# Optimization experiments

Hardware: AMD Instinct MI355X
Metric: run time of the kernel (lower is better)

## Reference

```python
import jax, jax.numpy as jnp
import numpy as np

H_MODEL = 1024
N_HEADS = 16
N_KV_HEADS = 4
HEAD_DIM = 64
SLIDING_WINDOW = 512
B, S = 2, 2048
NEG_INF = -1e9


def rotate_half(x):
    half = x.shape[-1] // 2
    return jnp.concatenate([-x[..., half:], x[..., :half]], axis=-1)


def setup_inputs() -> dict:
    key = jax.random.key(0)
    ks = jax.random.split(key, 8)
    hidden_states = jax.random.normal(ks[0], (B, S, H_MODEL), dtype=jnp.float32)
    # RoPE tables (HF style): cos/sin of shape [1, S, head_dim]
    inv_freq = 1.0 / (10000.0 ** (jnp.arange(0, HEAD_DIM, 2, dtype=jnp.float32) / HEAD_DIM))
    pos = jnp.arange(S, dtype=jnp.float32)
    freqs = jnp.einsum('s,d->sd', pos, inv_freq)            # [S, D/2]
    emb = jnp.concatenate([freqs, freqs], axis=-1)          # [S, D]
    cos = jnp.cos(emb)[None]                                # [1, S, D]
    sin = jnp.sin(emb)[None]
    # additive causal + sliding-window mask [1,1,S,S]
    i = jnp.arange(S)[:, None]
    j = jnp.arange(S)[None, :]
    allowed = (j <= i) & (i - j < SLIDING_WINDOW)
    attention_mask = jnp.where(allowed, 0.0, NEG_INF).astype(jnp.float32)[None, None]
    # projection weights (torch Linear stores [out, in]; y = x @ W.T)
    std = 0.02
    Wq = jax.random.normal(ks[1], (N_HEADS * HEAD_DIM, H_MODEL), dtype=jnp.float32) * std
    Wk = jax.random.normal(ks[2], (N_KV_HEADS * HEAD_DIM, H_MODEL), dtype=jnp.float32) * std
    Wv = jax.random.normal(ks[3], (N_KV_HEADS * HEAD_DIM, H_MODEL), dtype=jnp.float32) * std
    Wo = jax.random.normal(ks[4], (H_MODEL, N_HEADS * HEAD_DIM), dtype=jnp.float32) * std
    return {"hidden_states": hidden_states, "cos": cos, "sin": sin,
            "attention_mask": attention_mask, "Wq": Wq, "Wk": Wk, "Wv": Wv, "Wo": Wo}


def reference(hidden_states, cos, sin, attention_mask, Wq, Wk, Wv, Wo):
    b, s, _ = hidden_states.shape
    G = N_HEADS // N_KV_HEADS
    scaling = HEAD_DIM ** -0.5
    # QKV projections -> [B, H, S, D]
    q = jnp.einsum('bsh,oh->bso', hidden_states, Wq).reshape(b, s, N_HEADS, HEAD_DIM).transpose(0, 2, 1, 3)
    k = jnp.einsum('bsh,oh->bso', hidden_states, Wk).reshape(b, s, N_KV_HEADS, HEAD_DIM).transpose(0, 2, 1, 3)
    v = jnp.einsum('bsh,oh->bso', hidden_states, Wv).reshape(b, s, N_KV_HEADS, HEAD_DIM).transpose(0, 2, 1, 3)
    # RoPE (cos/sin broadcast over head dim via unsqueeze(1))
    c = cos[:, None, :, :]
    sn = sin[:, None, :, :]
    q = q * c + rotate_half(q) * sn
    k = k * c + rotate_half(k) * sn
    # GQA eager attention: group query heads over kv heads
    qg = q.reshape(b, N_KV_HEADS, G, s, HEAD_DIM)
    scores = jnp.einsum('bkgqd,bkpd->bkgqp', qg, k) * scaling  # [B,Hkv,G,S,S]
    scores = scores + attention_mask[:, :, None, :, :]
    probs = jax.nn.softmax(scores.astype(jnp.float32), axis=-1).astype(q.dtype)
    out = jnp.einsum('bkgqp,bkpd->bkgqd', probs, v)            # [B,Hkv,G,S,D]
    out = out.reshape(b, N_HEADS, s, HEAD_DIM).transpose(0, 2, 1, 3).reshape(b, s, N_HEADS * HEAD_DIM)
    return jnp.einsum('bso,ho->bsh', out, Wo)
```

## Files before the change

### kernel.cpp

```cpp
#include <hip/hip_runtime.h>
#include <hip/hip_bf16.h>

#define S_LEN 2048
#define NH 16
#define NKV 4
#define HD 64
#define WIN 512
#define BATCH 2

typedef __bf16 bf16_8 __attribute__((ext_vector_type(8)));
typedef __bf16 bf16_4 __attribute__((ext_vector_type(4)));
typedef float f32x4 __attribute__((ext_vector_type(4)));

__device__ inline void gld16(const __bf16* g, __bf16* l) {
    __builtin_amdgcn_global_load_lds(
        (const __attribute__((address_space(1))) void*)g,
        (__attribute__((address_space(3))) void*)l, 16, 0, 0);
}

__device__ inline bf16_8 cvt8(f32x4 a, f32x4 b) {
    bf16_8 r;
    r[0] = (__bf16)a[0]; r[1] = (__bf16)a[1]; r[2] = (__bf16)a[2]; r[3] = (__bf16)a[3];
    r[4] = (__bf16)b[0]; r[5] = (__bf16)b[1]; r[6] = (__bf16)b[2]; r[7] = (__bf16)b[3];
    return r;
}

__global__ __launch_bounds__(256) void cvt_w(
    const float* __restrict__ s0, const float* __restrict__ s1,
    const float* __restrict__ s2, const float* __restrict__ s3,
    __bf16* __restrict__ d0, __bf16* __restrict__ d1,
    __bf16* __restrict__ d2, __bf16* __restrict__ d3,
    int c0, int c1, int c2, int c3)
{
    const int i = blockIdx.x * blockDim.x + threadIdx.x;
    if (i >= c3) return;
    const float* s; __bf16* d; int base;
    if (i < c0)      { s = s0; d = d0; base = 0;  }
    else if (i < c1) { s = s1; d = d1; base = c0; }
    else if (i < c2) { s = s2; d = d2; base = c1; }
    else             { s = s3; d = d3; base = c2; }
    const size_t j = (size_t)(i - base) * 4;
    const f32x4 v = *(const f32x4*)(s + j);
    bf16_4 o;
    o[0] = (__bf16)v[0]; o[1] = (__bf16)v[1];
    o[2] = (__bf16)v[2]; o[3] = (__bf16)v[3];
    *(bf16_4*)(d + j) = o;
}

__global__ __launch_bounds__(256) void gemm_qkv(
    const float* __restrict__ A,
    const __bf16* __restrict__ Wqb,
    const __bf16* __restrict__ Wkb,
    const __bf16* __restrict__ Wvb,
    __bf16* __restrict__ Qb,
    __bf16* __restrict__ Kb,
    __bf16* __restrict__ Vt,
    const float* __restrict__ cosb,
    const float* __restrict__ sinb)
{
    __shared__ __align__(16) __bf16 As[64 * 32];
    __shared__ __align__(16) __bf16 Bs[128 * 32];

    const int tid  = threadIdx.x;
    const int wave = tid >> 6;
    const int lane = tid & 63;
    const int wm   = wave & 1;
    const int wn   = wave >> 1;

    const int row0 = blockIdx.x * 64;
    const int by   = blockIdx.y;

    const __bf16* B; int colb; int mode;
    __bf16* C; int ldc; int col0;
    if (by < 8)       { B = Wqb; colb = by * 128;        C = Qb; ldc = 1024; col0 = by * 128;        mode = 0; }
    else if (by < 10) { B = Wkb; colb = (by - 8) * 128;  C = Kb; ldc = 256;  col0 = (by - 8) * 128;  mode = 1; }
    else              { B = Wvb; colb = (by - 10) * 128; C = 0;  ldc = 0;    col0 = (by - 10) * 128; mode = 2; }

    const int arow = tid >> 2;
    const int akc  = (tid & 3) << 3;
    const int srow = lane >> 2;
    const int skc  = (lane & 3) << 3;

    const int fm = lane & 15;
    const int fk = (lane >> 4) << 3;

    const f32x4 fzero = {0.f, 0.f, 0.f, 0.f};
    f32x4 acc[2][4];
#pragma unroll
    for (int i = 0; i < 2; ++i)
#pragma unroll
        for (int nt = 0; nt < 4; ++nt) acc[i][nt] = fzero;

    for (int k0 = 0; k0 < 1024; k0 += 32) {
        const f32x4 x0 = *(const f32x4*)&A[(size_t)(row0 + arow) * 1024 + k0 + akc];
        const f32x4 x1 = *(const f32x4*)&A[(size_t)(row0 + arow) * 1024 + k0 + akc + 4];
#pragma unroll
        for (int s = 0; s < 2; ++s) {
            const int ch = 2 * wave + s;
            gld16(&B[(size_t)(colb + ch * 16 + srow) * 1024 + k0 + skc],
                  &Bs[ch * 16 * 32]);
        }
        *(bf16_8*)&As[arow * 32 + akc] = cvt8(x0, x1);
        __syncthreads();

        bf16_8 af[2], bfr[4];
#pragma unroll
        for (int i = 0; i < 2; ++i)
            af[i] = *(const bf16_8*)&As[(wm * 32 + i * 16 + fm) * 32 + fk];
#pragma unroll
        for (int nt = 0; nt < 4; ++nt)
            bfr[nt] = *(const bf16_8*)&Bs[(wn * 64 + nt * 16 + fm) * 32 + fk];
#pragma unroll
        for (int i = 0; i < 2; ++i)
#pragma unroll
            for (int nt = 0; nt < 4; ++nt)
                acc[i][nt] = __builtin_amdgcn_mfma_f32_16x16x32_bf16(af[i], bfr[nt], acc[i][nt], 0, 0, 0);
        __syncthreads();
    }

    const int drow = (lane >> 4) << 2;
    const int cq   = col0 + wn * 64;
    if (mode < 2) {
#pragma unroll
        for (int i = 0; i < 2; ++i) {
#pragma unroll
            for (int r = 0; r < 4; ++r) {
                const int row = row0 + wm * 32 + i * 16 + drow + r;
                const int s   = row & (S_LEN - 1);
#pragma unroll
                for (int nt = 0; nt < 2; ++nt) {
                    const int d = nt * 16 + fm;
                    const float c1 = cosb[s * HD + d];
                    const float s1 = sinb[s * HD + d];
                    const float c2 = cosb[s * HD + d + 32];
                    const float s2 = sinb[s * HD + d + 32];
                    const float x1 = acc[i][nt][r];
                    const float x2 = acc[i][nt + 2][r];
                    C[(size_t)row * ldc + cq + d]      = (__bf16)(x1 * c1 - x2 * s1);
                    C[(size_t)row * ldc + cq + d + 32] = (__bf16)(x2 * c2 + x1 * s2);
                }
            }
        }
    } else {
        const int kh = cq >> 6;
#pragma unroll
        for (int i = 0; i < 2; ++i) {
#pragma unroll
            for (int r = 0; r < 4; ++r) {
                const int row = row0 + wm * 32 + i * 16 + drow + r;
                const int b   = row >> 11;
                const int s   = row & (S_LEN - 1);
#pragma unroll
                for (int nt = 0; nt < 4; ++nt) {
                    const int d = nt * 16 + fm;
                    Vt[(size_t)((b * NKV + kh) * HD + d) * S_LEN + s] = (__bf16)acc[i][nt][r];
                }
            }
        }
    }
}

__global__ __launch_bounds__(256) void gemm_o(
    const __bf16* __restrict__ A,
    const __bf16* __restrict__ B,
    float* __restrict__ C)
{
    __shared__ __align__(16) __bf16 As[64 * 32];
    __shared__ __align__(16) __bf16 Bs[128 * 32];

    const int tid  = threadIdx.x;
    const int wave = tid >> 6;
    const int lane = tid & 63;
    const int wm   = wave & 1;
    const int wn   = wave >> 1;

    const int row0 = blockIdx.x * 64;
    const int colb = blockIdx.y * 128;

    const int srow = lane >> 2;
    const int skc  = (lane & 3) << 3;
    const int fm = lane & 15;
    const int fk = (lane >> 4) << 3;

    const f32x4 fzero = {0.f, 0.f, 0.f, 0.f};
    f32x4 acc[2][4];
#pragma unroll
    for (int i = 0; i < 2; ++i)
#pragma unroll
        for (int nt = 0; nt < 4; ++nt) acc[i][nt] = fzero;

    const int ch0 = wave * 3;
    for (int k0 = 0; k0 < 1024; k0 += 32) {
#pragma unroll
        for (int t = 0; t < 3; ++t) {
            const int ch = ch0 + t;
            if (ch < 4)
                gld16(&A[(size_t)(row0 + ch * 16 + srow) * 1024 + k0 + skc],
                      &As[ch * 16 * 32]);
            else
                gld16(&B[(size_t)(colb + (ch - 4) * 16 + srow) * 1024 + k0 + skc],
                      &Bs[(ch - 4) * 16 * 32]);
        }
        __syncthreads();

        bf16_8 af[2], bfr[4];
#pragma unroll
        for (int i = 0; i < 2; ++i)
            af[i] = *(const bf16_8*)&As[(wm * 32 + i * 16 + fm) * 32 + fk];
#pragma unroll
        for (int nt = 0; nt < 4; ++nt)
            bfr[nt] = *(const bf16_8*)&Bs[(wn * 64 + nt * 16 + fm) * 32 + fk];
#pragma unroll
        for (int i = 0; i < 2; ++i)
#pragma unroll
            for (int nt = 0; nt < 4; ++nt)
                acc[i][nt] = __builtin_amdgcn_mfma_f32_16x16x32_bf16(af[i], bfr[nt], acc[i][nt], 0, 0, 0);
        __syncthreads();
    }

    const int drow = (lane >> 4) << 2;
#pragma unroll
    for (int i = 0; i < 2; ++i)
#pragma unroll
        for (int r = 0; r < 4; ++r) {
            const int row = row0 + wm * 32 + i * 16 + drow + r;
#pragma unroll
            for (int nt = 0; nt < 4; ++nt)
                C[(size_t)row * 1024 + colb + wn * 64 + nt * 16 + fm] = acc[i][nt][r];
        }
}

__global__ __launch_bounds__(256) void attn_mfma(const __bf16* __restrict__ Q,
                                                 const __bf16* __restrict__ K,
                                                 const __bf16* __restrict__ Vt,
                                                 __bf16* __restrict__ O)
{
    __shared__ __align__(16) __bf16 Ks[32][72];
    __shared__ __align__(16) __bf16 Vs[64][40];
    __shared__ __align__(16) __bf16 Ps[4][16][40];

    const int tid  = threadIdx.x;
    const int wave = tid >> 6;
    const int lane = tid & 63;

    const int qt = blockIdx.x & (S_LEN / 64 - 1);
    const int h  = (blockIdx.x >> 5) & (NH - 1);
    const int b  = blockIdx.x >> 9;
    const int kh = h >> 2;

    const int q0 = qt * 64;
    const int qw = q0 + wave * 16;

    const int fm = lane & 15;
    const int fj = (lane >> 4) << 3;

    const size_t qrow = (size_t)(b * S_LEN + qw + fm) * (NH * HD) + h * HD;
    const bf16_8 qf0 = *(const bf16_8*)&Q[qrow + fj];
    const bf16_8 qf1 = *(const bf16_8*)&Q[qrow + 32 + fj];

    const f32x4 fzero = {0.f, 0.f, 0.f, 0.f};
    f32x4 oacc[4];
    float l[4];
#pragma unroll
    for (int nt = 0; nt < 4; ++nt) oacc[nt] = fzero;
#pragma unroll
    for (int r = 0; r < 4; ++r) l[r] = 0.f;

    const int skr = tid >> 3;
    const int skc = (tid & 7) << 3;
    const int svd = tid >> 2;
    const int svj = (tid & 3) << 3;

    const size_t vrow = (size_t)((b * NKV + kh) * HD + svd) * S_LEN;
    const int qbase = qw + ((lane >> 4) << 2);

    const int lo = (q0 >= WIN) ? (q0 - WIN) : 0;

    for (int kb = lo; kb <= q0 + 32; kb += 32) {
        __syncthreads();
        *(bf16_8*)&Ks[skr][skc] =
            *(const bf16_8*)&K[(size_t)(b * S_LEN + kb + skr) * (NKV * HD) + kh * HD + skc];
        *(bf16_8*)&Vs[svd][svj] = *(const bf16_8*)&Vt[vrow + kb + svj];
        __syncthreads();

        if (kb <= qw + 15 && (qw - kb) < (WIN + 31)) {
            f32x4 s0 = fzero, s1 = fzero;
            {
                const bf16_8 k00 = *(const bf16_8*)&Ks[fm][fj];
                const bf16_8 k01 = *(const bf16_8*)&Ks[fm][32 + fj];
                const bf16_8 k10 = *(const bf16_8*)&Ks[16 + fm][fj];
                const bf16_8 k11 = *(const bf16_8*)&Ks[16 + fm][32 + fj];
                s0 = __builtin_amdgcn_mfma_f32_16x16x32_bf16(qf0, k00, s0, 0, 0, 0);
                s0 = __builtin_amdgcn_mfma_f32_16x16x32_bf16(qf1, k01, s0, 0, 0, 0);
                s1 = __builtin_amdgcn_mfma_f32_16x16x32_bf16(qf0, k10, s1, 0, 0, 0);
                s1 = __builtin_amdgcn_mfma_f32_16x16x32_bf16(qf1, k11, s1, 0, 0, 0);
            }

            float p0[4], p1[4];
            const int k0i = kb + fm;
            const int k1i = kb + 16 + fm;
#pragma unroll
            for (int r = 0; r < 4; ++r) {
                const int qr = qbase + r;
                const float e0 = __expf(s0[r] * 0.125f);
                const float e1 = __expf(s1[r] * 0.125f);
                p0[r] = (k0i <= qr && qr - k0i < WIN) ? e0 : 0.f;
                p1[r] = (k1i <= qr && qr - k1i < WIN) ? e1 : 0.f;
                l[r] += p0[r] + p1[r];
            }

#pragma unroll
            for (int r = 0; r < 4; ++r) {
                Ps[wave][((lane >> 4) << 2) + r][fm]      = (__bf16)p0[r];
                Ps[wave][((lane >> 4) << 2) + r][16 + fm] = (__bf16)p1[r];
            }

            const bf16_8 pf = *(const bf16_8*)&Ps[wave][fm][fj];
#pragma unroll
            for (int nt = 0; nt < 4; ++nt) {
                const bf16_8 vf = *(const bf16_8*)&Vs[nt * 16 + fm][fj];
                oacc[nt] = __builtin_amdgcn_mfma_f32_16x16x32_bf16(pf, vf, oacc[nt], 0, 0, 0);
            }
        }
    }

#pragma unroll
    for (int off = 8; off > 0; off >>= 1)
#pragma unroll
        for (int r = 0; r < 4; ++r)
            l[r] += __shfl_xor(l[r], off, 64);

    const int drow = (lane >> 4) << 2;
    float inv[4];
#pragma unroll
    for (int r = 0; r < 4; ++r) inv[r] = 1.0f / l[r];
#pragma unroll
    for (int nt = 0; nt < 4; ++nt)
#pragma unroll
        for (int r = 0; r < 4; ++r) {
            const size_t off = (size_t)(b * S_LEN + qw + drow + r) * (NH * HD) + h * HD + nt * 16 + fm;
            O[off] = (__bf16)(oacc[nt][r] * inv[r]);
        }
}

extern "C" void kernel_launch(void* const* d_in, const int* in_sizes, int n_in,
                              void* d_out, int out_size, void* d_ws, size_t ws_size,
                              hipStream_t stream)
{
    const float* hs   = (const float*)d_in[0];
    const float* cosb = (const float*)d_in[1];
    const float* sinb = (const float*)d_in[2];
    const float* Wq = (const float*)d_in[4];
    const float* Wk = (const float*)d_in[5];
    const float* Wv = (const float*)d_in[6];
    const float* Wo = (const float*)d_in[7];

    const int M = BATCH * S_LEN;

    __bf16* Wqb = (__bf16*)d_ws;
    __bf16* Wkb = Wqb + 1024 * 1024;
    __bf16* Wvb = Wkb + 256 * 1024;
    __bf16* Wob = Wvb + 256 * 1024;
    __bf16* Qb  = Wob + 1024 * 1024;
    __bf16* Kb  = Qb  + (size_t)M * 1024;
    __bf16* Vtb = Kb  + (size_t)M * 256;
    __bf16* Ob  = Vtb + (size_t)M * 256;

    const int c0 = 262144;
    const int c1 = c0 + 65536;
    const int c2 = c1 + 65536;
    const int c3 = c2 + 262144;

    dim3 blk(256);
    cvt_w<<<(c3 + 255) / 256, blk, 0, stream>>>(Wq, Wk, Wv, Wo,
                                                Wqb, Wkb, Wvb, Wob,
                                                c0, c1, c2, c3);

    gemm_qkv<<<dim3(64, 12), blk, 0, stream>>>(hs, Wqb, Wkb, Wvb,
                                               Qb, Kb, Vtb, cosb, sinb);

    attn_mfma<<<BATCH * NH * (S_LEN / 64), blk, 0, stream>>>(Qb, Kb, Vtb, Ob);

    gemm_o<<<dim3(64, 8), blk, 0, stream>>>(Ob, Wob, (float*)d_out);
}
```

Measured before the change: 175.6 us.

## Double-buffer LDS tiles in GEMMs and attention, stage V transpose through LDS

Adds double-buffered shared-memory tiles to the QKV GEMM, the output GEMM and the attention kernel. The next K-slice's global loads are issued before the current MFMA work, and the previous trailing barrier is removed. This is meant to hide global load latency behind compute. The V projection epilogue now transposes through LDS so Vt is written with contiguous 16-byte stores instead of scattered 2-byte stores, at the cost of more shared memory per block and possibly lower occupancy.

```diff
diff --git a/kernel.cpp b/kernel.cpp
--- a/kernel.cpp
+++ b/kernel.cpp
@@ -58,8 +58,9 @@
     const float* __restrict__ cosb,
     const float* __restrict__ sinb)
 {
-    __shared__ __align__(16) __bf16 As[64 * 32];
-    __shared__ __align__(16) __bf16 Bs[128 * 32];
+    __shared__ __align__(16) __bf16 smem[12288];
+    __bf16* const AsB = smem;
+    __bf16* const BsB = smem + 4096;
 
     const int tid  = threadIdx.x;
     const int wave = tid >> 6;
@@ -91,30 +92,51 @@
 #pragma unroll
         for (int nt = 0; nt < 4; ++nt) acc[i][nt] = fzero;
 
-    for (int k0 = 0; k0 < 1024; k0 += 32) {
-        const f32x4 x0 = *(const f32x4*)&A[(size_t)(row0 + arow) * 1024 + k0 + akc];
-        const f32x4 x1 = *(const f32x4*)&A[(size_t)(row0 + arow) * 1024 + k0 + akc + 4];
+    const size_t aoff = (size_t)(row0 + arow) * 1024 + akc;
+
+    {
+        const f32x4 x0 = *(const f32x4*)&A[aoff];
+        const f32x4 x1 = *(const f32x4*)&A[aoff + 4];
 #pragma unroll
         for (int s = 0; s < 2; ++s) {
             const int ch = 2 * wave + s;
-            gld16(&B[(size_t)(colb + ch * 16 + srow) * 1024 + k0 + skc],
-                  &Bs[ch * 16 * 32]);
-        }
-        *(bf16_8*)&As[arow * 32 + akc] = cvt8(x0, x1);
-        __syncthreads();
+            gld16(&B[(size_t)(colb + ch * 16 + srow) * 1024 + skc], &BsB[ch * 16 * 32]);
+        }
+        *(bf16_8*)&AsB[arow * 32 + akc] = cvt8(x0, x1);
+    }
+    __syncthreads();
+
+    for (int it = 0; it < 32; ++it) {
+        const int cur = it & 1;
+        const int nxt = cur ^ 1;
+        const bool pf = (it + 1) < 32;
+        f32x4 x0, x1;
+        if (pf) {
+            const int k0 = (it + 1) << 5;
+            x0 = *(const f32x4*)&A[aoff + k0];
+            x1 = *(const f32x4*)&A[aoff + k0 + 4];
+#pragma unroll
+            for (int s = 0; s < 2; ++s) {
+                const int ch = 2 * wave + s;
+                gld16(&B[(size_t)(colb + ch * 16 + srow) * 1024 + k0 + skc],
+                      &BsB[nxt * 4096 + ch * 16 * 32]);
+            }
+        }
 
         bf16_8 af[2], bfr[4];
 #pragma unroll
         for (int i = 0; i < 2; ++i)
-            af[i] = *(const bf16_8*)&As[(wm * 32 + i * 16 + fm) * 32 + fk];
+            af[i] = *(const bf16_8*)&AsB[cur * 2048 + (wm * 32 + i * 16 + fm) * 32 + fk];
 #pragma unroll
         for (int nt = 0; nt < 4; ++nt)
-            bfr[nt] = *(const bf16_8*)&Bs[(wn * 64 + nt * 16 + fm) * 32 + fk];
+            bfr[nt] = *(const bf16_8*)&BsB[cur * 4096 + (wn * 64 + nt * 16 + fm) * 32 + fk];
 #pragma unroll
         for (int i = 0; i < 2; ++i)
 #pragma unroll
             for (int nt = 0; nt < 4; ++nt)
                 acc[i][nt] = __builtin_amdgcn_mfma_f32_16x16x32_bf16(af[i], bfr[nt], acc[i][nt], 0, 0, 0);
+
+        if (pf) *(bf16_8*)&AsB[nxt * 2048 + arow * 32 + akc] = cvt8(x0, x1);
         __syncthreads();
     }
 
@@ -142,21 +164,25 @@
             }
         }
     } else {
-        const int kh = cq >> 6;
-#pragma unroll
-        for (int i = 0; i < 2; ++i) {
-#pragma unroll
-            for (int r = 0; r < 4; ++r) {
-                const int row = row0 + wm * 32 + i * 16 + drow + r;
-                const int b   = row >> 11;
-                const int s   = row & (S_LEN - 1);
-#pragma unroll
-                for (int nt = 0; nt < 4; ++nt) {
-                    const int d = nt * 16 + fm;
-                    Vt[(size_t)((b * NKV + kh) * HD + d) * S_LEN + s] = (__bf16)acc[i][nt][r];
-                }
-            }
-        }
+        __bf16* T = smem;
+#pragma unroll
+        for (int i = 0; i < 2; ++i)
+#pragma unroll
+            for (int r = 0; r < 4; ++r)
+#pragma unroll
+                for (int nt = 0; nt < 4; ++nt)
+                    T[(wn * 64 + nt * 16 + fm) * 72 + wm * 32 + i * 16 + drow + r] =
+                        (__bf16)acc[i][nt][r];
+        __syncthreads();
+        const int nl = tid >> 1;
+        const int so = (tid & 1) << 5;
+        const int ng = col0 + nl;
+        const int kh = ng >> 6, d = ng & 63;
+        const int b  = row0 >> 11, s0v = row0 & (S_LEN - 1);
+        __bf16* dst = &Vt[(size_t)((b * NKV + kh) * HD + d) * S_LEN + s0v + so];
+#pragma unroll
+        for (int c = 0; c < 4; ++c)
+            *(bf16_8*)(dst + c * 8) = *(const bf16_8*)&T[nl * 72 + so + c * 8];
     }
 }
 
@@ -165,8 +191,9 @@
     const __bf16* __restrict__ B,
     float* __restrict__ C)
 {
-    __shared__ __align__(16) __bf16 As[64 * 32];
-    __shared__ __align__(16) __bf16 Bs[128 * 32];
+    __shared__ __align__(16) __bf16 smem[12288];
+    __bf16* const AsB = smem;
+    __bf16* const BsB = smem + 4096;
 
     const int tid  = threadIdx.x;
     const int wave = tid >> 6;
@@ -190,26 +217,41 @@
         for (int nt = 0; nt < 4; ++nt) acc[i][nt] = fzero;
 
     const int ch0 = wave * 3;
-    for (int k0 = 0; k0 < 1024; k0 += 32) {
-#pragma unroll
-        for (int t = 0; t < 3; ++t) {
-            const int ch = ch0 + t;
-            if (ch < 4)
-                gld16(&A[(size_t)(row0 + ch * 16 + srow) * 1024 + k0 + skc],
-                      &As[ch * 16 * 32]);
-            else
-                gld16(&B[(size_t)(colb + (ch - 4) * 16 + srow) * 1024 + k0 + skc],
-                      &Bs[(ch - 4) * 16 * 32]);
-        }
-        __syncthreads();
+
+#pragma unroll
+    for (int t = 0; t < 3; ++t) {
+        const int ch = ch0 + t;
+        if (ch < 4)
+            gld16(&A[(size_t)(row0 + ch * 16 + srow) * 1024 + skc], &AsB[ch * 16 * 32]);
+        else
+            gld16(&B[(size_t)(colb + (ch - 4) * 16 + srow) * 1024 + skc], &BsB[(ch - 4) * 16 * 32]);
+    }
+    __syncthreads();
+
+    for (int it = 0; it < 32; ++it) {
+        const int cur = it & 1;
+        const int nxt = cur ^ 1;
+        if (it + 1 < 32) {
+            const int k0 = (it + 1) << 5;
+#pragma unroll
+            for (int t = 0; t < 3; ++t) {
+                const int ch = ch0 + t;
+                if (ch < 4)
+                    gld16(&A[(size_t)(row0 + ch * 16 + srow) * 1024 + k0 + skc],
+                          &AsB[nxt * 2048 + ch * 16 * 32]);
+                else
+                    gld16(&B[(size_t)(colb + (ch - 4) * 16 + srow) * 1024 + k0 + skc],
+                          &BsB[nxt * 4096 + (ch - 4) * 16 * 32]);
+            }
+        }
 
         bf16_8 af[2], bfr[4];
 #pragma unroll
         for (int i = 0; i < 2; ++i)
-            af[i] = *(const bf16_8*)&As[(wm * 32 + i * 16 + fm) * 32 + fk];
+            af[i] = *(const bf16_8*)&AsB[cur * 2048 + (wm * 32 + i * 16 + fm) * 32 + fk];
 #pragma unroll
         for (int nt = 0; nt < 4; ++nt)
-            bfr[nt] = *(const bf16_8*)&Bs[(wn * 64 + nt * 16 + fm) * 32 + fk];
+            bfr[nt] = *(const bf16_8*)&BsB[cur * 4096 + (wn * 64 + nt * 16 + fm) * 32 + fk];
 #pragma unroll
         for (int i = 0; i < 2; ++i)
 #pragma unroll
@@ -235,8 +277,8 @@
                                                  const __bf16* __restrict__ Vt,
                                                  __bf16* __restrict__ O)
 {
-    __shared__ __align__(16) __bf16 Ks[32][72];
-    __shared__ __align__(16) __bf16 Vs[64][40];
+    __shared__ __align__(16) __bf16 Ks[2][32][72];
+    __shared__ __align__(16) __bf16 Vs[2][64][40];
     __shared__ __align__(16) __bf16 Ps[4][16][40];
 
     const int tid  = threadIdx.x;
@@ -271,25 +313,38 @@
     const int svd = tid >> 2;
     const int svj = (tid & 3) << 3;
 
-    const size_t vrow = (size_t)((b * NKV + kh) * HD + svd) * S_LEN;
+    const size_t krow = (size_t)(b * S_LEN + skr) * (NKV * HD) + kh * HD + skc;
+    const size_t vrow = (size_t)((b * NKV + kh) * HD + svd) * S_LEN + svj;
     const int qbase = qw + ((lane >> 4) << 2);
 
-    const int lo = (q0 >= WIN) ? (q0 - WIN) : 0;
-
-    for (int kb = lo; kb <= q0 + 32; kb += 32) {
-        __syncthreads();
-        *(bf16_8*)&Ks[skr][skc] =
-            *(const bf16_8*)&K[(size_t)(b * S_LEN + kb + skr) * (NKV * HD) + kh * HD + skc];
-        *(bf16_8*)&Vs[svd][svj] = *(const bf16_8*)&Vt[vrow + kb + svj];
-        __syncthreads();
+    const int lo  = (q0 >= WIN) ? (q0 - WIN) : 0;
+    const int nit = ((q0 + 32 - lo) >> 5) + 1;
+
+    {
+        const bf16_8 kr = *(const bf16_8*)&K[krow + (size_t)lo * (NKV * HD)];
+        const bf16_8 vr = *(const bf16_8*)&Vt[vrow + lo];
+        *(bf16_8*)&Ks[0][skr][skc] = kr;
+        *(bf16_8*)&Vs[0][svd][svj] = vr;
+    }
+    __syncthreads();
+
+    for (int it = 0; it < nit; ++it) {
+        const int kb  = lo + (it << 5);
+        const int cur = it & 1;
+        const bool pf = (it + 1) < nit;
+        bf16_8 kr, vr;
+        if (pf) {
+            kr = *(const bf16_8*)&K[krow + (size_t)(kb + 32) * (NKV * HD)];
+            vr = *(const bf16_8*)&Vt[vrow + kb + 32];
+        }
 
         if (kb <= qw + 15 && (qw - kb) < (WIN + 31)) {
             f32x4 s0 = fzero, s1 = fzero;
             {
-                const bf16_8 k00 = *(const bf16_8*)&Ks[fm][fj];
-                const bf16_8 k01 = *(const bf16_8*)&Ks[fm][32 + fj];
-                const bf16_8 k10 = *(const bf16_8*)&Ks[16 + fm][fj];
-                const bf16_8 k11 = *(const bf16_8*)&Ks[16 + fm][32 + fj];
+                const bf16_8 k00 = *(const bf16_8*)&Ks[cur][fm][fj];
+                const bf16_8 k01 = *(const bf16_8*)&Ks[cur][fm][32 + fj];
+                const bf16_8 k10 = *(const bf16_8*)&Ks[cur][16 + fm][fj];
+                const bf16_8 k11 = *(const bf16_8*)&Ks[cur][16 + fm][32 + fj];
                 s0 = __builtin_amdgcn_mfma_f32_16x16x32_bf16(qf0, k00, s0, 0, 0, 0);
                 s0 = __builtin_amdgcn_mfma_f32_16x16x32_bf16(qf1, k01, s0, 0, 0, 0);
                 s1 = __builtin_amdgcn_mfma_f32_16x16x32_bf16(qf0, k10, s1, 0, 0, 0);
@@ -315,13 +370,19 @@
                 Ps[wave][((lane >> 4) << 2) + r][16 + fm] = (__bf16)p1[r];
             }
 
-            const bf16_8 pf = *(const bf16_8*)&Ps[wave][fm][fj];
+            const bf16_8 pf8 = *(const bf16_8*)&Ps[wave][fm][fj];
 #pragma unroll
             for (int nt = 0; nt < 4; ++nt) {
-                const bf16_8 vf = *(const bf16_8*)&Vs[nt * 16 + fm][fj];
-                oacc[nt] = __builtin_amdgcn_mfma_f32_16x16x32_bf16(pf, vf, oacc[nt], 0, 0, 0);
-            }
-        }
+                const bf16_8 vf = *(const bf16_8*)&Vs[cur][nt * 16 + fm][fj];
+                oacc[nt] = __builtin_amdgcn_mfma_f32_16x16x32_bf16(pf8, vf, oacc[nt], 0, 0, 0);
+            }
+        }
+
+        if (pf) {
+            *(bf16_8*)&Ks[cur ^ 1][skr][skc] = kr;
+            *(bf16_8*)&Vs[cur ^ 1][svd][svj] = vr;
+        }
+        __syncthreads();
     }
 
 #pragma unroll
```

Measured after the change: 168.9 us. -3.8%, faster.
